# Performance work log

Measured on AMD Instinct MI355X. Metric: run time of the kernel, lower is better.

## Reference

```python
import jax, jax.numpy as jnp
import numpy as np

H = 64
N = 200000
E = 2000000
EPS = 1e-5


def layernorm(x, g, b):
    mu = jnp.mean(x, axis=-1, keepdims=True)
    var = jnp.var(x, axis=-1, keepdims=True)
    return (x - mu) * jax.lax.rsqrt(var + EPS) * g + b


def setup_inputs() -> dict:
    key = jax.random.key(0)
    ks = jax.random.split(key, 12)
    s = 0.02
    return {
        "z": jax.random.normal(ks[0], (N, H), dtype=jnp.float32),
        "pot_arcs": jax.random.randint(ks[1], (E, 2), 0, N + 1, dtype=jnp.int64),
        "root_w": jax.random.normal(ks[2], (H, 1), dtype=jnp.float32) * s,
        "root_b": jax.random.normal(ks[3], (H,), dtype=jnp.float32) * s,
        "lin1_w": jax.random.normal(ks[4], (H, H), dtype=jnp.float32) * s,
        "lin1_b": jax.random.normal(ks[5], (H,), dtype=jnp.float32) * s,
        "lin2_w": jax.random.normal(ks[6], (H, H), dtype=jnp.float32) * s,
        "lin2_b": jax.random.normal(ks[7], (H,), dtype=jnp.float32) * s,
        "bil_w": jax.random.normal(ks[8], (1, H, H), dtype=jnp.float32) * s,
        "bil_b": jax.random.normal(ks[9], (1,), dtype=jnp.float32) * s,
        "norm_g": jnp.ones((H,), dtype=jnp.float32),
        "norm_b": jnp.zeros((H,), dtype=jnp.float32),
    }


def reference(z, pot_arcs, root_w, root_b, lin1_w, lin1_b, lin2_w, lin2_b,
              bil_w, bil_b, norm_g, norm_b):
    # root feature: Linear(1->H) applied to ones((1,1)) => root_w[:,0] + root_b
    root_feat = (root_w[:, 0] + root_b)[None, :]           # [1, H]
    zz = jnp.concatenate([root_feat, z], axis=0)           # [N+1, H]
    zz = layernorm(zz, norm_g, norm_b)

    # edge gather (irregular access)
    h1 = zz[pot_arcs[:, 0]]                                # [E, H]
    h2 = zz[pot_arcs[:, 1]]                                # [E, H]

    # dual linear -> relu -> LayerNorm (dropout = identity in eval)
    x1 = layernorm(jax.nn.relu(h1 @ lin1_w.T + lin1_b), norm_g, norm_b)
    x2 = layernorm(jax.nn.relu(h2 @ lin2_w.T + lin2_b), norm_g, norm_b)

    # bilinear score: x1 @ W[0] @ x2 per edge, +b
    score = jnp.einsum('eh,hg,eg->e', x1, bil_w[0], x2) + bil_b[0]
    return score                                            # [E]
```

## Files before the change

kernel.cpp:

```cpp
#include <hip/hip_runtime.h>
#include <hip/hip_bf16.h>

typedef unsigned short u16;
typedef unsigned int u32;

typedef float f32x4 __attribute__((ext_vector_type(4)));
typedef short bf16x8 __attribute__((ext_vector_type(8)));

#define HDIM 64
#define EPS 1e-5f
#define XROW 68


__device__ __forceinline__ float wave_sum64(float v) {
    v += __shfl_xor(v, 1, 64);
    v += __shfl_xor(v, 2, 64);
    v += __shfl_xor(v, 4, 64);
    v += __shfl_xor(v, 8, 64);
    v += __shfl_xor(v, 16, 64);
    v += __shfl_xor(v, 32, 64);
    return v;
}

__device__ __forceinline__ float bcast(float v, int k) {
    return __int_as_float(__builtin_amdgcn_readlane(__float_as_int(v), k));
}

__device__ __forceinline__ u16 f2bf(float f) {
    u32 u = __float_as_uint(f);
    u32 r = (u + 0x7fffu + ((u >> 16) & 1u)) >> 16;
    return (u16)r;
}

__device__ __forceinline__ float bflo(u32 w) { return __uint_as_float(w << 16); }
__device__ __forceinline__ float bfhi(u32 w) { return __uint_as_float(w & 0xffff0000u); }

__global__ __launch_bounds__(256) void prep_kernel(
    const float* __restrict__ lin1_w, const float* __restrict__ lin2_w,
    const float* __restrict__ bil_w,
    u16* __restrict__ w1bf, u16* __restrict__ w2bf, u16* __restrict__ btbf)
{
    const int tid = threadIdx.x;
    for (int i = tid; i < 4096; i += 256) {
        w1bf[i] = f2bf(lin1_w[i]);
        w2bf[i] = f2bf(lin2_w[i]);
        const int g = i >> 6, h = i & 63;
        btbf[i] = f2bf(bil_w[h * 64 + g]);
    }
}

__device__ __forceinline__ bf16x8 load_afrag(const u16* Xs, int l, int s) {
    const int row = l & 15;
    const int k0  = 8 * (l >> 4) + 32 * s;
    union { uint2 u[2]; bf16x8 f; } c;
    c.u[0] = *(const uint2*)&Xs[row * XROW + k0];
    c.u[1] = *(const uint2*)&Xs[row * XROW + k0 + 4];
    return c.f;
}

__device__ __forceinline__ bf16x8 load_bfrag(const u16* __restrict__ W,
                                             int l, int t, int s) {
    const int n  = (l & 15) + 16 * t;
    const int k0 = 8 * (l >> 4) + 32 * s;
    return *(const bf16x8*)&W[n * 64 + k0];
}

__device__ __forceinline__ void relu_ln_acc(f32x4* acc, const float* biasv,
                                            const float* gv, const float* bvv) {
    float s[4] = {0.f,0.f,0.f,0.f}, q[4] = {0.f,0.f,0.f,0.f};
#pragma unroll
    for (int t = 0; t < 4; ++t)
#pragma unroll
        for (int j = 0; j < 4; ++j) {
            float v = fmaxf(acc[t][j] + biasv[t], 0.f);
            acc[t][j] = v;
            s[j] += v; q[j] = fmaf(v, v, q[j]);
        }
#pragma unroll
    for (int j = 0; j < 4; ++j) {
#pragma unroll
        for (int m = 1; m < 16; m <<= 1) {
            s[j] += __shfl_xor(s[j], m, 64);
            q[j] += __shfl_xor(q[j], m, 64);
        }
        const float mu = s[j] * 0.015625f;
        const float rs = rsqrtf(q[j] * 0.015625f - mu * mu + EPS);
#pragma unroll
        for (int t = 0; t < 4; ++t)
            acc[t][j] = (acc[t][j] - mu) * rs * gv[t] + bvv[t];
    }
}

__device__ __forceinline__ void acc_to_lds(u16* Y, const f32x4* acc, int l) {
    const int hcol = l & 15;
#pragma unroll
    for (int j = 0; j < 4; ++j) {
        const int row = (l >> 4) * 4 + j;
#pragma unroll
        for (int t = 0; t < 4; ++t)
            Y[row * XROW + hcol + 16 * t] = f2bf(acc[t][j]);
    }
}

__device__ __forceinline__ void lds_to_global(u16* __restrict__ T, const u16* Y,
                                              int l, int n0, int nnodes) {
    const int row  = l >> 2;
    const int node = n0 + row;
    if (node < nnodes) {
        const int co = (l & 3) * 16;
        uint2 p0 = *(const uint2*)&Y[row * XROW + co];
        uint2 p1 = *(const uint2*)&Y[row * XROW + co + 4];
        uint2 p2 = *(const uint2*)&Y[row * XROW + co + 8];
        uint2 p3 = *(const uint2*)&Y[row * XROW + co + 12];
        uint4* d = (uint4*)(T + (size_t)node * HDIM + co);
        d[0] = make_uint4(p0.x, p0.y, p1.x, p1.y);
        d[1] = make_uint4(p2.x, p2.y, p3.x, p3.y);
    }
}

__global__ __launch_bounds__(256) void phase1_kernel(
    const float* __restrict__ z,
    const float* __restrict__ root_w, const float* __restrict__ root_b,
    const u16* __restrict__ w1bf, const float* __restrict__ lin1_b,
    const u16* __restrict__ w2bf, const float* __restrict__ lin2_b,
    const u16* __restrict__ btbf,
    const float* __restrict__ norm_g, const float* __restrict__ norm_b,
    u16* __restrict__ T1, u16* __restrict__ T2, int nnodes)
{
    __shared__ u16 XsAll[4][16 * XROW];
    __shared__ u16 YsAll[4][16 * XROW];

    const int tid = threadIdx.x;
    const int wid = tid >> 6;
    const int l   = tid & 63;
    u16* Xs = XsAll[wid];
    u16* Ys = YsAll[wid];

    const int n0 = (blockIdx.x * 4 + wid) * 16;

    {
        const int row  = l >> 2;
        const int node = n0 + row;
        const int c0   = (l & 3) * 16;
        float r[16];
        if (node == 0) {
#pragma unroll
            for (int qq = 0; qq < 4; ++qq) {
                const float4 a = *(const float4*)&root_w[c0 + 4*qq];
                const float4 b = *(const float4*)&root_b[c0 + 4*qq];
                r[4*qq] = a.x + b.x; r[4*qq+1] = a.y + b.y;
                r[4*qq+2] = a.z + b.z; r[4*qq+3] = a.w + b.w;
            }
        } else if (node < nnodes) {
            const float4* zp = (const float4*)(z + (size_t)(node - 1) * HDIM + c0);
#pragma unroll
            for (int qq = 0; qq < 4; ++qq) {
                const float4 v = zp[qq];
                r[4*qq] = v.x; r[4*qq+1] = v.y; r[4*qq+2] = v.z; r[4*qq+3] = v.w;
            }
        } else {
#pragma unroll
            for (int k = 0; k < 16; ++k) r[k] = 0.f;
        }
        float s = 0.f, sq = 0.f;
#pragma unroll
        for (int k = 0; k < 16; ++k) { s += r[k]; sq = fmaf(r[k], r[k], sq); }
        s  += __shfl_xor(s, 1, 64);  sq += __shfl_xor(sq, 1, 64);
        s  += __shfl_xor(s, 2, 64);  sq += __shfl_xor(sq, 2, 64);
        const float mu = s * 0.015625f;
        const float rs = rsqrtf(sq * 0.015625f - mu * mu + EPS);
        u16 tmp[16];
#pragma unroll
        for (int qq = 0; qq < 4; ++qq) {
            const float4 g4 = *(const float4*)&norm_g[c0 + 4*qq];
            const float4 b4 = *(const float4*)&norm_b[c0 + 4*qq];
            tmp[4*qq]   = f2bf((r[4*qq]   - mu) * rs * g4.x + b4.x);
            tmp[4*qq+1] = f2bf((r[4*qq+1] - mu) * rs * g4.y + b4.y);
            tmp[4*qq+2] = f2bf((r[4*qq+2] - mu) * rs * g4.z + b4.z);
            tmp[4*qq+3] = f2bf((r[4*qq+3] - mu) * rs * g4.w + b4.w);
        }
        u16* dst = &Xs[row * XROW + c0];
#pragma unroll
        for (int j = 0; j < 4; ++j)
            *(uint2*)&dst[4*j] = *(const uint2*)&tmp[4*j];
    }

    const int hcol = l & 15;
    float gv[4], bv[4], b1v[4], b2v[4];
#pragma unroll
    for (int t = 0; t < 4; ++t) {
        gv[t]  = norm_g[hcol + 16*t];
        bv[t]  = norm_b[hcol + 16*t];
        b1v[t] = lin1_b[hcol + 16*t];
        b2v[t] = lin2_b[hcol + 16*t];
    }

    bf16x8 a0 = load_afrag(Xs, l, 0);
    bf16x8 a1 = load_afrag(Xs, l, 1);

    f32x4 acc2[4], acc1[4];
#pragma unroll
    for (int t = 0; t < 4; ++t) {
        f32x4 c = {0.f, 0.f, 0.f, 0.f};
        c = __builtin_amdgcn_mfma_f32_16x16x32_bf16(a0, load_bfrag(w2bf, l, t, 0), c, 0, 0, 0);
        c = __builtin_amdgcn_mfma_f32_16x16x32_bf16(a1, load_bfrag(w2bf, l, t, 1), c, 0, 0, 0);
        acc2[t] = c;
    }
#pragma unroll
    for (int t = 0; t < 4; ++t) {
        f32x4 c = {0.f, 0.f, 0.f, 0.f};
        c = __builtin_amdgcn_mfma_f32_16x16x32_bf16(a0, load_bfrag(w1bf, l, t, 0), c, 0, 0, 0);
        c = __builtin_amdgcn_mfma_f32_16x16x32_bf16(a1, load_bfrag(w1bf, l, t, 1), c, 0, 0, 0);
        acc1[t] = c;
    }

    relu_ln_acc(acc2, b2v, gv, bv);
    acc_to_lds(Ys, acc2, l);
    lds_to_global(T2, Ys, l, n0, nnodes);

    relu_ln_acc(acc1, b1v, gv, bv);
    acc_to_lds(Xs, acc1, l);
    a0 = load_afrag(Xs, l, 0);
    a1 = load_afrag(Xs, l, 1);

    f32x4 acc3[4];
#pragma unroll
    for (int t = 0; t < 4; ++t) {
        f32x4 c = {0.f, 0.f, 0.f, 0.f};
        c = __builtin_amdgcn_mfma_f32_16x16x32_bf16(a0, load_bfrag(btbf, l, t, 0), c, 0, 0, 0);
        c = __builtin_amdgcn_mfma_f32_16x16x32_bf16(a1, load_bfrag(btbf, l, t, 1), c, 0, 0, 0);
        acc3[t] = c;
    }
    acc_to_lds(Ys, acc3, l);
    lds_to_global(T1, Ys, l, n0, nnodes);
}

__global__ __launch_bounds__(256) void phase2_kernel(
    const int* __restrict__ arcs,
    const u16* __restrict__ T1, const u16* __restrict__ T2,
    const float* __restrict__ bil_b,
    float* __restrict__ out, int E)
{
    const int tid = blockIdx.x * 256 + threadIdx.x;
    const int e = tid >> 3;
    if (e >= E) return;
    const int l8 = tid & 7;

    const int i0 = arcs[2 * e];
    const int i1 = arcs[2 * e + 1];

    const uint4* p1 = (const uint4*)(T1 + (size_t)i0 * HDIM) + l8;
    const uint4* p2 = (const uint4*)(T2 + (size_t)i1 * HDIM) + l8;
    uint4 u = *p1;
    uint4 v = *p2;

    float s = 0.f;
    {
        u32 ua[4] = {u.x, u.y, u.z, u.w};
        u32 va[4] = {v.x, v.y, v.z, v.w};
#pragma unroll
        for (int i = 0; i < 4; ++i) {
            s = fmaf(bflo(ua[i]), bflo(va[i]), s);
            s = fmaf(bfhi(ua[i]), bfhi(va[i]), s);
        }
    }
    s += __shfl_xor(s, 1, 64);
    s += __shfl_xor(s, 2, 64);
    s += __shfl_xor(s, 4, 64);
    if (l8 == 0) out[e] = s + bil_b[0];
}

__device__ __forceinline__ float lnorm_w(float v, float g, float b) {
    float mu = wave_sum64(v) * 0.015625f;
    float d  = v - mu;
    float var = wave_sum64(d * d) * 0.015625f;
    return d * rsqrtf(var + EPS) * g + b;
}

__global__ __launch_bounds__(256) void edge_direct_kernel(
    const float* __restrict__ z, const int* __restrict__ arcs,
    const float* __restrict__ root_w, const float* __restrict__ root_b,
    const float* __restrict__ lin1_w, const float* __restrict__ lin1_b,
    const float* __restrict__ lin2_w, const float* __restrict__ lin2_b,
    const float* __restrict__ bil_w, const float* __restrict__ bil_b,
    const float* __restrict__ norm_g, const float* __restrict__ norm_b,
    float* __restrict__ out, int E, int nnodes)
{
    __shared__ float W1t[4096], W2t[4096], Bs[4096];
    const int tid = threadIdx.x;
    for (int i = tid; i < 4096; i += 256) {
        int h = i >> 6, k = i & 63;
        W1t[(k << 6) | h] = lin1_w[i];
        W2t[(k << 6) | h] = lin2_w[i];
        Bs[i] = bil_w[i];
    }
    __syncthreads();

    const int lane = tid & 63;
    const float g  = norm_g[lane], bt = norm_b[lane];
    const float b1 = lin1_b[lane], b2 = lin2_b[lane];
    const float rootv = root_w[lane] + root_b[lane];

    const int gwave = (blockIdx.x * 256 + tid) >> 6;
    const int nwaves = (gridDim.x * 256) >> 6;

    for (int e = gwave; e < E; e += nwaves) {
        int i0 = arcs[2 * e], i1 = arcs[2 * e + 1];
        float v0 = (i0 == 0) ? rootv : z[(size_t)(i0 - 1) * HDIM + lane];
        float v1 = (i1 == 0) ? rootv : z[(size_t)(i1 - 1) * HDIM + lane];
        float l0 = lnorm_w(v0, g, bt);
        float l1 = lnorm_w(v1, g, bt);
        float a1 = 0.f, a2 = 0.f;
#pragma unroll
        for (int k = 0; k < 64; ++k) {
            a1 = fmaf(bcast(l0, k), W1t[(k << 6) | lane], a1);
            a2 = fmaf(bcast(l1, k), W2t[(k << 6) | lane], a2);
        }
        float x1 = lnorm_w(fmaxf(a1 + b1, 0.f), g, bt);
        float x2 = lnorm_w(fmaxf(a2 + b2, 0.f), g, bt);
        float w1 = 0.f;
#pragma unroll
        for (int h = 0; h < 64; ++h)
            w1 = fmaf(bcast(x1, h), Bs[(h << 6) | lane], w1);
        float sc = wave_sum64(w1 * x2);
        if (lane == 0) out[e] = sc + bil_b[0];
    }
}

extern "C" void kernel_launch(void* const* d_in, const int* in_sizes, int n_in,
                              void* d_out, int out_size, void* d_ws, size_t ws_size,
                              hipStream_t stream) {
    const float* z      = (const float*)d_in[0];
    const int*   arcs   = (const int*)  d_in[1];
    const float* root_w = (const float*)d_in[2];
    const float* root_b = (const float*)d_in[3];
    const float* lin1_w = (const float*)d_in[4];
    const float* lin1_b = (const float*)d_in[5];
    const float* lin2_w = (const float*)d_in[6];
    const float* lin2_b = (const float*)d_in[7];
    const float* bil_w  = (const float*)d_in[8];
    const float* bil_b  = (const float*)d_in[9];
    const float* norm_g = (const float*)d_in[10];
    const float* norm_b = (const float*)d_in[11];
    float* out = (float*)d_out;

    const int E      = in_sizes[1] / 2;
    const int nnodes = in_sizes[0] / HDIM + 1;

    const size_t tbl  = (size_t)nnodes * HDIM * sizeof(u16);
    const size_t need = 2 * tbl + 3 * 4096 * sizeof(u16);

    if (ws_size >= need) {
        u16* T1   = (u16*)d_ws;
        u16* T2   = (u16*)((char*)d_ws + tbl);
        u16* w1bf = (u16*)((char*)d_ws + 2 * tbl);
        u16* w2bf = w1bf + 4096;
        u16* btbf = w2bf + 4096;

        prep_kernel<<<1, 256, 0, stream>>>(lin1_w, lin2_w, bil_w, w1bf, w2bf, btbf);

        const int blocks1 = (nnodes + 63) / 64;
        phase1_kernel<<<blocks1, 256, 0, stream>>>(
            z, root_w, root_b, w1bf, lin1_b, w2bf, lin2_b, btbf,
            norm_g, norm_b, T1, T2, nnodes);

        const long long thr2 = (long long)E * 8;
        const int blocks2 = (int)((thr2 + 255) / 256);
        phase2_kernel<<<blocks2, 256, 0, stream>>>(arcs, T1, T2, bil_b, out, E);
    } else {
        edge_direct_kernel<<<8192, 256, 0, stream>>>(
            z, arcs, root_w, root_b, lin1_w, lin1_b, lin2_w, lin2_b,
            bil_w, bil_b, norm_g, norm_b, out, E, nnodes);
    }
}
```

Measured before the change: 131.7 us.

## Process 32 nodes per wave in phase1 and two edges per lane group in phase2

Phase1 now tiles 32 nodes per wave, so each loaded weight B-fragment is reused across two MFMA row tiles. The separate Y scratch buffer is dropped by reusing Xs, and global writes are done with wider per-lane stores. Phase2 handles two edges per 8-lane group to put more independent gathers in flight, and its output uses nontemporal stores. The cost is more registers (32-float row buffer, doubled accumulators) and half as many blocks, which may reduce occupancy.

```diff
diff --git a/kernel.cpp b/kernel.cpp
--- a/kernel.cpp
+++ b/kernel.cpp
@@ -49,8 +49,8 @@
     }
 }
 
-__device__ __forceinline__ bf16x8 load_afrag(const u16* Xs, int l, int s) {
-    const int row = l & 15;
+__device__ __forceinline__ bf16x8 load_afrag(const u16* Xs, int l, int m, int s) {
+    const int row = 16 * m + (l & 15);
     const int k0  = 8 * (l >> 4) + 32 * s;
     union { uint2 u[2]; bf16x8 f; } c;
     c.u[0] = *(const uint2*)&Xs[row * XROW + k0];
@@ -91,31 +91,32 @@
     }
 }
 
-__device__ __forceinline__ void acc_to_lds(u16* Y, const f32x4* acc, int l) {
+__device__ __forceinline__ void acc_to_lds(u16* Xs, const f32x4* acc, int l, int m) {
     const int hcol = l & 15;
 #pragma unroll
     for (int j = 0; j < 4; ++j) {
-        const int row = (l >> 4) * 4 + j;
+        const int row = 16 * m + (l >> 4) * 4 + j;
 #pragma unroll
         for (int t = 0; t < 4; ++t)
-            Y[row * XROW + hcol + 16 * t] = f2bf(acc[t][j]);
-    }
-}
-
-__device__ __forceinline__ void lds_to_global(u16* __restrict__ T, const u16* Y,
-                                              int l, int n0, int nnodes) {
-    const int row  = l >> 2;
+            Xs[row * XROW + hcol + 16 * t] = f2bf(acc[t][j]);
+    }
+}
+
+__device__ __forceinline__ void lds_to_global32(u16* __restrict__ T, const u16* Xs,
+                                                int l, int n0, int nnodes) {
+    const int row  = l >> 1;
     const int node = n0 + row;
-    if (node < nnodes) {
-        const int co = (l & 3) * 16;
-        uint2 p0 = *(const uint2*)&Y[row * XROW + co];
-        uint2 p1 = *(const uint2*)&Y[row * XROW + co + 4];
-        uint2 p2 = *(const uint2*)&Y[row * XROW + co + 8];
-        uint2 p3 = *(const uint2*)&Y[row * XROW + co + 12];
-        uint4* d = (uint4*)(T + (size_t)node * HDIM + co);
-        d[0] = make_uint4(p0.x, p0.y, p1.x, p1.y);
-        d[1] = make_uint4(p2.x, p2.y, p3.x, p3.y);
-    }
+    if (node >= nnodes) return;
+    const int c0 = (l & 1) * 32;
+    const u16* src = &Xs[row * XROW + c0];
+    uint2 p[8];
+#pragma unroll
+    for (int j = 0; j < 8; ++j) p[j] = *(const uint2*)&src[4*j];
+    uint4* d = (uint4*)(T + (size_t)node * HDIM + c0);
+    d[0] = make_uint4(p[0].x, p[0].y, p[1].x, p[1].y);
+    d[1] = make_uint4(p[2].x, p[2].y, p[3].x, p[3].y);
+    d[2] = make_uint4(p[4].x, p[4].y, p[5].x, p[5].y);
+    d[3] = make_uint4(p[6].x, p[6].y, p[7].x, p[7].y);
 }
 
 __global__ __launch_bounds__(256) void phase1_kernel(
@@ -127,25 +128,23 @@
     const float* __restrict__ norm_g, const float* __restrict__ norm_b,
     u16* __restrict__ T1, u16* __restrict__ T2, int nnodes)
 {
-    __shared__ u16 XsAll[4][16 * XROW];
-    __shared__ u16 YsAll[4][16 * XROW];
+    __shared__ u16 XsAll[4][32 * XROW];
 
     const int tid = threadIdx.x;
     const int wid = tid >> 6;
     const int l   = tid & 63;
     u16* Xs = XsAll[wid];
-    u16* Ys = YsAll[wid];
-
-    const int n0 = (blockIdx.x * 4 + wid) * 16;
+
+    const int n0 = (blockIdx.x * 4 + wid) * 32;
 
     {
-        const int row  = l >> 2;
+        const int row  = l >> 1;
         const int node = n0 + row;
-        const int c0   = (l & 3) * 16;
-        float r[16];
+        const int c0   = (l & 1) * 32;
+        float r[32];
         if (node == 0) {
 #pragma unroll
-            for (int qq = 0; qq < 4; ++qq) {
+            for (int qq = 0; qq < 8; ++qq) {
                 const float4 a = *(const float4*)&root_w[c0 + 4*qq];
                 const float4 b = *(const float4*)&root_b[c0 + 4*qq];
                 r[4*qq] = a.x + b.x; r[4*qq+1] = a.y + b.y;
@@ -154,35 +153,34 @@
         } else if (node < nnodes) {
             const float4* zp = (const float4*)(z + (size_t)(node - 1) * HDIM + c0);
 #pragma unroll
-            for (int qq = 0; qq < 4; ++qq) {
+            for (int qq = 0; qq < 8; ++qq) {
                 const float4 v = zp[qq];
                 r[4*qq] = v.x; r[4*qq+1] = v.y; r[4*qq+2] = v.z; r[4*qq+3] = v.w;
             }
         } else {
 #pragma unroll
-            for (int k = 0; k < 16; ++k) r[k] = 0.f;
+            for (int k = 0; k < 32; ++k) r[k] = 0.f;
         }
         float s = 0.f, sq = 0.f;
 #pragma unroll
-        for (int k = 0; k < 16; ++k) { s += r[k]; sq = fmaf(r[k], r[k], sq); }
+        for (int k = 0; k < 32; ++k) { s += r[k]; sq = fmaf(r[k], r[k], sq); }
         s  += __shfl_xor(s, 1, 64);  sq += __shfl_xor(sq, 1, 64);
-        s  += __shfl_xor(s, 2, 64);  sq += __shfl_xor(sq, 2, 64);
         const float mu = s * 0.015625f;
         const float rs = rsqrtf(sq * 0.015625f - mu * mu + EPS);
-        u16 tmp[16];
-#pragma unroll
-        for (int qq = 0; qq < 4; ++qq) {
+        u16* dst = &Xs[row * XROW + c0];
+#pragma unroll
+        for (int qq = 0; qq < 8; ++qq) {
             const float4 g4 = *(const float4*)&norm_g[c0 + 4*qq];
             const float4 b4 = *(const float4*)&norm_b[c0 + 4*qq];
-            tmp[4*qq]   = f2bf((r[4*qq]   - mu) * rs * g4.x + b4.x);
-            tmp[4*qq+1] = f2bf((r[4*qq+1] - mu) * rs * g4.y + b4.y);
-            tmp[4*qq+2] = f2bf((r[4*qq+2] - mu) * rs * g4.z + b4.z);
-            tmp[4*qq+3] = f2bf((r[4*qq+3] - mu) * rs * g4.w + b4.w);
-        }
-        u16* dst = &Xs[row * XROW + c0];
-#pragma unroll
-        for (int j = 0; j < 4; ++j)
-            *(uint2*)&dst[4*j] = *(const uint2*)&tmp[4*j];
+            u16 t0 = f2bf((r[4*qq]   - mu) * rs * g4.x + b4.x);
+            u16 t1 = f2bf((r[4*qq+1] - mu) * rs * g4.y + b4.y);
+            u16 t2 = f2bf((r[4*qq+2] - mu) * rs * g4.z + b4.z);
+            u16 t3 = f2bf((r[4*qq+3] - mu) * rs * g4.w + b4.w);
+            uint2 pw;
+            pw.x = (u32)t0 | ((u32)t1 << 16);
+            pw.y = (u32)t2 | ((u32)t3 << 16);
+            *(uint2*)&dst[4*qq] = pw;
+        }
     }
 
     const int hcol = l & 15;
@@ -195,44 +193,80 @@
         b2v[t] = lin2_b[hcol + 16*t];
     }
 
-    bf16x8 a0 = load_afrag(Xs, l, 0);
-    bf16x8 a1 = load_afrag(Xs, l, 1);
-
-    f32x4 acc2[4], acc1[4];
+    bf16x8 a[2][2];
+#pragma unroll
+    for (int m = 0; m < 2; ++m) {
+        a[m][0] = load_afrag(Xs, l, m, 0);
+        a[m][1] = load_afrag(Xs, l, m, 1);
+    }
+
+    f32x4 acc2[2][4], acc1[2][4];
 #pragma unroll
     for (int t = 0; t < 4; ++t) {
-        f32x4 c = {0.f, 0.f, 0.f, 0.f};
-        c = __builtin_amdgcn_mfma_f32_16x16x32_bf16(a0, load_bfrag(w2bf, l, t, 0), c, 0, 0, 0);
-        c = __builtin_amdgcn_mfma_f32_16x16x32_bf16(a1, load_bfrag(w2bf, l, t, 1), c, 0, 0, 0);
-        acc2[t] = c;
+        const bf16x8 b0 = load_bfrag(w2bf, l, t, 0);
+        const bf16x8 b1 = load_bfrag(w2bf, l, t, 1);
+#pragma unroll
+        for (int m = 0; m < 2; ++m) {
+            f32x4 c = {0.f, 0.f, 0.f, 0.f};
+            c = __builtin_amdgcn_mfma_f32_16x16x32_bf16(a[m][0], b0, c, 0, 0, 0);
+            c = __builtin_amdgcn_mfma_f32_16x16x32_bf16(a[m][1], b1, c, 0, 0, 0);
+            acc2[m][t] = c;
+        }
     }
 #pragma unroll
     for (int t = 0; t < 4; ++t) {
-        f32x4 c = {0.f, 0.f, 0.f, 0.f};
-        c = __builtin_amdgcn_mfma_f32_16x16x32_bf16(a0, load_bfrag(w1bf, l, t, 0), c, 0, 0, 0);
-        c = __builtin_amdgcn_mfma_f32_16x16x32_bf16(a1, load_bfrag(w1bf, l, t, 1), c, 0, 0, 0);
-        acc1[t] = c;
-    }
-
-    relu_ln_acc(acc2, b2v, gv, bv);
-    acc_to_lds(Ys, acc2, l);
-    lds_to_global(T2, Ys, l, n0, nnodes);
-
-    relu_ln_acc(acc1, b1v, gv, bv);
-    acc_to_lds(Xs, acc1, l);
-    a0 = load_afrag(Xs, l, 0);
-    a1 = load_afrag(Xs, l, 1);
-
-    f32x4 acc3[4];
+        const bf16x8 b0 = load_bfrag(w1bf, l, t, 0);
+        const bf16x8 b1 = load_bfrag(w1bf, l, t, 1);
+#pragma unroll
+        for (int m = 0; m < 2; ++m) {
+            f32x4 c = {0.f, 0.f, 0.f, 0.f};
+            c = __builtin_amdgcn_mfma_f32_16x16x32_bf16(a[m][0], b0, c, 0, 0, 0);
+            c = __builtin_amdgcn_mfma_f32_16x16x32_bf16(a[m][1], b1, c, 0, 0, 0);
+            acc1[m][t] = c;
+        }
+    }
+
+    relu_ln_acc(acc2[0], b2v, gv, bv);
+    relu_ln_acc(acc2[1], b2v, gv, bv);
+    acc_to_lds(Xs, acc2[0], l, 0);
+    acc_to_lds(Xs, acc2[1], l, 1);
+    lds_to_global32(T2, Xs, l, n0, nnodes);
+
+    relu_ln_acc(acc1[0], b1v, gv, bv);
+    relu_ln_acc(acc1[1], b1v, gv, bv);
+    acc_to_lds(Xs, acc1[0], l, 0);
+    acc_to_lds(Xs, acc1[1], l, 1);
+#pragma unroll
+    for (int m = 0; m < 2; ++m) {
+        a[m][0] = load_afrag(Xs, l, m, 0);
+        a[m][1] = load_afrag(Xs, l, m, 1);
+    }
+
+    f32x4 acc3[2][4];
 #pragma unroll
     for (int t = 0; t < 4; ++t) {
-        f32x4 c = {0.f, 0.f, 0.f, 0.f};
-        c = __builtin_amdgcn_mfma_f32_16x16x32_bf16(a0, load_bfrag(btbf, l, t, 0), c, 0, 0, 0);
-        c = __builtin_amdgcn_mfma_f32_16x16x32_bf16(a1, load_bfrag(btbf, l, t, 1), c, 0, 0, 0);
-        acc3[t] = c;
-    }
-    acc_to_lds(Ys, acc3, l);
-    lds_to_global(T1, Ys, l, n0, nnodes);
+        const bf16x8 b0 = load_bfrag(btbf, l, t, 0);
+        const bf16x8 b1 = load_bfrag(btbf, l, t, 1);
+#pragma unroll
+        for (int m = 0; m < 2; ++m) {
+            f32x4 c = {0.f, 0.f, 0.f, 0.f};
+            c = __builtin_amdgcn_mfma_f32_16x16x32_bf16(a[m][0], b0, c, 0, 0, 0);
+            c = __builtin_amdgcn_mfma_f32_16x16x32_bf16(a[m][1], b1, c, 0, 0, 0);
+            acc3[m][t] = c;
+        }
+    }
+    acc_to_lds(Xs, acc3[0], l, 0);
+    acc_to_lds(Xs, acc3[1], l, 1);
+    lds_to_global32(T1, Xs, l, n0, nnodes);
+}
+
+__device__ __forceinline__ float dot8(uint4 u, uint4 v) {
+    float s = 0.f;
+    s = fmaf(bflo(u.x), bflo(v.x), s); s = fmaf(bfhi(u.x), bfhi(v.x), s);
+    s = fmaf(bflo(u.y), bflo(v.y), s); s = fmaf(bfhi(u.y), bfhi(v.y), s);
+    s = fmaf(bflo(u.z), bflo(v.z), s); s = fmaf(bfhi(u.z), bfhi(v.z), s);
+    s = fmaf(bflo(u.w), bflo(v.w), s); s = fmaf(bfhi(u.w), bfhi(v.w), s);
+    return s;
 }
 
 __global__ __launch_bounds__(256) void phase2_kernel(
@@ -241,33 +275,39 @@
     const float* __restrict__ bil_b,
     float* __restrict__ out, int E)
 {
-    const int tid = blockIdx.x * 256 + threadIdx.x;
-    const int e = tid >> 3;
-    if (e >= E) return;
-    const int l8 = tid & 7;
-
-    const int i0 = arcs[2 * e];
-    const int i1 = arcs[2 * e + 1];
-
-    const uint4* p1 = (const uint4*)(T1 + (size_t)i0 * HDIM) + l8;
-    const uint4* p2 = (const uint4*)(T2 + (size_t)i1 * HDIM) + l8;
-    uint4 u = *p1;
-    uint4 v = *p2;
-
-    float s = 0.f;
-    {
-        u32 ua[4] = {u.x, u.y, u.z, u.w};
-        u32 va[4] = {v.x, v.y, v.z, v.w};
-#pragma unroll
-        for (int i = 0; i < 4; ++i) {
-            s = fmaf(bflo(ua[i]), bflo(va[i]), s);
-            s = fmaf(bfhi(ua[i]), bfhi(va[i]), s);
-        }
-    }
-    s += __shfl_xor(s, 1, 64);
-    s += __shfl_xor(s, 2, 64);
-    s += __shfl_xor(s, 4, 64);
-    if (l8 == 0) out[e] = s + bil_b[0];
+    const int gtid = blockIdx.x * 256 + threadIdx.x;
+    const int wv = gtid >> 6;
+    const int l  = gtid & 63;
+    const int l8 = l & 7;
+    const int le = l >> 3;
+    const int e0 = wv * 16 + le;
+    const int e1 = e0 + 8;
+    const bool ok0 = e0 < E, ok1 = e1 < E;
+
+    uint4 u0, v0, u1, v1;
+    if (ok0) {
+        const int i0 = arcs[2 * e0], j0 = arcs[2 * e0 + 1];
+        u0 = *((const uint4*)(T1 + (size_t)i0 * HDIM) + l8);
+        v0 = *((const uint4*)(T2 + (size_t)j0 * HDIM) + l8);
+    }
+    if (ok1) {
+        const int i1 = arcs[2 * e1], j1 = arcs[2 * e1 + 1];
+        u1 = *((const uint4*)(T1 + (size_t)i1 * HDIM) + l8);
+        v1 = *((const uint4*)(T2 + (size_t)j1 * HDIM) + l8);
+    }
+
+    float s0 = ok0 ? dot8(u0, v0) : 0.f;
+    float s1 = ok1 ? dot8(u1, v1) : 0.f;
+
+    s0 += __shfl_xor(s0, 1, 64);  s1 += __shfl_xor(s1, 1, 64);
+    s0 += __shfl_xor(s0, 2, 64);  s1 += __shfl_xor(s1, 2, 64);
+    s0 += __shfl_xor(s0, 4, 64);  s1 += __shfl_xor(s1, 4, 64);
+
+    if (l8 == 0) {
+        const float bb = bil_b[0];
+        if (ok0) __builtin_nontemporal_store(s0 + bb, &out[e0]);
+        if (ok1) __builtin_nontemporal_store(s1 + bb, &out[e1]);
+    }
 }
 
 __device__ __forceinline__ float lnorm_w(float v, float g, float b) {
@@ -359,12 +399,12 @@
 
         prep_kernel<<<1, 256, 0, stream>>>(lin1_w, lin2_w, bil_w, w1bf, w2bf, btbf);
 
-        const int blocks1 = (nnodes + 63) / 64;
+        const int blocks1 = (nnodes + 127) / 128;
         phase1_kernel<<<blocks1, 256, 0, stream>>>(
             z, root_w, root_b, w1bf, lin1_b, w2bf, lin2_b, btbf,
             norm_g, norm_b, T1, T2, nnodes);
 
-        const long long thr2 = (long long)E * 8;
+        const long long thr2 = (long long)E * 4;
         const int blocks2 = (int)((thr2 + 255) / 256);
         phase2_kernel<<<blocks2, 256, 0, stream>>>(arcs, T1, T2, bil_b, out, E);
     } else {
```

New measurement: 132.6 us. No clear change (+0.7%).
